# Kernel optimization log

Hardware: AMD Instinct MI355X
Metric: run time of the kernel (lower is better)

The kernel has to match this reference:

```python
import jax, jax.numpy as jnp
import numpy as np
import math
from itertools import combinations

SEQ_LEN = 8
D_MODEL = 2048
OUT_DIM = 1152
WAY = 5
SHOT = 5
N_SUPPORT = WAY * SHOT
N_QUERIES = 200
TUPLES = np.array(list(combinations(range(SEQ_LEN), 2)), dtype=np.int32)  # [28, 2]
L = TUPLES.shape[0]  # 28 temporal tuples
PE_SCALE = 0.1
LN_EPS = 1e-5
COS_EPS = 1e-8


def _pos_encoding(seq, d):
    pos = jnp.arange(seq, dtype=jnp.float32)[:, None]
    div = jnp.exp(jnp.arange(0, d, 2, dtype=jnp.float32) * (-math.log(10000.0) / d))
    pe = jnp.zeros((seq, d), dtype=jnp.float32)
    pe = pe.at[:, 0::2].set(jnp.sin(pos * div) * PE_SCALE)
    pe = pe.at[:, 1::2].set(jnp.cos(pos * div) * PE_SCALE)
    return pe  # [seq, d]


def _layernorm(x, g, b):
    mu = x.mean(-1, keepdims=True)
    var = ((x - mu) ** 2).mean(-1, keepdims=True)
    return (x - mu) * jax.lax.rsqrt(var + LN_EPS) * g + b


def setup_inputs() -> dict:
    key = jax.random.key(0)
    ks = jax.random.split(key, 6)
    support_set = jax.random.normal(ks[0], (N_SUPPORT, SEQ_LEN, D_MODEL), jnp.float32)
    queries = jax.random.normal(ks[1], (N_QUERIES, SEQ_LEN, D_MODEL), jnp.float32)
    # sorted equal-shot episode: labels = [0]*5 + [1]*5 + ... + [4]*5
    support_labels = jnp.repeat(jnp.arange(WAY, dtype=jnp.int32), SHOT)
    k_w = jax.random.normal(ks[2], (OUT_DIM, 2 * D_MODEL), jnp.float32) * 0.02
    v_w = jax.random.normal(ks[3], (OUT_DIM, 2 * D_MODEL), jnp.float32) * 0.02
    k_b = jnp.zeros((OUT_DIM,), jnp.float32)
    v_b = jnp.zeros((OUT_DIM,), jnp.float32)
    ln_k_g = jnp.ones((OUT_DIM,), jnp.float32)
    ln_k_b = jnp.zeros((OUT_DIM,), jnp.float32)
    return {"support_set": support_set, "support_labels": support_labels,
            "queries": queries, "k_w": k_w, "k_b": k_b, "v_w": v_w, "v_b": v_b,
            "ln_k_g": ln_k_g, "ln_k_b": ln_k_b}


def reference(support_set, support_labels, queries, k_w, k_b, v_w, v_b, ln_k_g, ln_k_b):
    # dropout is inference-mode (identity)
    pe = _pos_encoding(SEQ_LEN, D_MODEL)
    sp = support_set + pe  # [Ns, S, D_MODEL]
    qp = queries + pe      # [Nq, S, D_MODEL]

    tup = jnp.asarray(TUPLES)
    # gather temporal tuples: [N, L, 2, D_MODEL] -> [N, L, 2*D_MODEL]
    s_t = sp[:, tup].reshape(N_SUPPORT, L, 2 * D_MODEL)
    q_t = qp[:, tup].reshape(N_QUERIES, L, 2 * D_MODEL)

    ks_s = _layernorm(s_t @ k_w.T + k_b, ln_k_g, ln_k_b)  # [Ns, L, OUT]
    ks_q = _layernorm(q_t @ k_w.T + k_b, ln_k_g, ln_k_b)  # [Nq, L, OUT]
    vs_s = s_t @ v_w.T + v_b                               # [Ns, L, OUT] (no norm, per original)
    vs_q = q_t @ v_w.T + v_b                               # [Nq, L, OUT]

    # labels are sorted equal-shot -> group by class via reshape
    ks_c = ks_s.reshape(WAY, SHOT, L, OUT_DIM)
    vs_c = vs_s.reshape(WAY, SHOT, L, OUT_DIM)

    # attention scores: [WAY, Nq, L(query tuple), SHOT, L(support tuple)]
    scores = jnp.einsum('qld,wsed->wqlse', ks_q, ks_c) / math.sqrt(OUT_DIM)
    attn = jax.nn.softmax(scores.reshape(WAY, N_QUERIES, L, SHOT * L), axis=-1)
    attn = attn.reshape(WAY, N_QUERIES, L, SHOT, L)
    # prototype: sum over shot of attn @ class_v -> [WAY, Nq, L, OUT]
    proto = jnp.einsum('wqlse,wsed->wqld', attn, vs_c)

    # query logits: -||q_v - proto||_F^2 / L per class
    diff = vs_q[None] - proto  # [WAY, Nq, L, OUT]
    ori = (-(diff ** 2).sum(axis=(-2, -1)) / L).T  # [Nq, WAY]

    # all_distances_tensor [Nq, L*OUT, WAY]
    A = jnp.transpose(proto, (1, 2, 3, 0)).reshape(N_QUERIES, L * OUT_DIM, WAY)
    num = jnp.einsum('qda,qdb->qab', A, A)            # [Nq, WAY, WAY]
    nrm = jnp.sqrt((A * A).sum(axis=1))               # [Nq, WAY]
    den = jnp.maximum(nrm[:, :, None] * nrm[:, None, :], COS_EPS)
    sim = num / den                                    # [Nq, WAY, WAY]
    return sim, ori
```

## Files before the change

kernel.cpp:

```cpp
#include <hip/hip_runtime.h>
#include <hip/hip_bf16.h>
#include <math.h>

typedef __hip_bfloat16 bf16;
typedef short s16x8 __attribute__((ext_vector_type(8)));
typedef float f32x4 __attribute__((ext_vector_type(4)));

#define NQ 200
#define SEQ 8
#define DM 2048
#define OUTD 1152
#define LT 28
#define M_ALL 6300
#define SM 5600
#define SN_PAD 768
#define ATT_STRIDE 720
#define N2 2304
#define KP 160
#define CH_Q 50
#define CH_ROWS 1400
#define CH_MPAD 1408
#define ABLK 144

__device__ __forceinline__ float bf2f(bf16 v) { return __bfloat162float(v); }
__device__ __forceinline__ bf16 f2bf(float v) { return __float2bfloat16(v); }
__device__ __forceinline__ float ubits2f(unsigned int u16) {
    unsigned int i = u16 << 16;
    float f; __builtin_memcpy(&f, &i, 4); return f;
}
__device__ __forceinline__ unsigned short f2bits(float f) {
    bf16 b = __float2bfloat16(f);
    unsigned short u; __builtin_memcpy(&u, &b, 2); return u;
}

__device__ const int TUP_A[LT] = {0,0,0,0,0,0,0,1,1,1,1,1,1,2,2,2,2,2,3,3,3,3,4,4,4,5,5,6};
__device__ const int TUP_B[LT] = {1,2,3,4,5,6,7,2,3,4,5,6,7,3,4,5,6,7,4,5,6,7,5,6,7,6,7,7};

__global__ __launch_bounds__(256) void wconv2_k(const float4* __restrict__ kw,
                                                const float4* __restrict__ vw,
                                                ushort4* __restrict__ o) {
    int i = blockIdx.x * 256 + threadIdx.x;
    float4 v = (i < 1179648) ? kw[i] : vw[i - 1179648];
    ushort4 r;
    r.x = f2bits(v.x); r.y = f2bits(v.y); r.z = f2bits(v.z); r.w = f2bits(v.w);
    o[i] = r;
}

__global__ __launch_bounds__(256) void pe_k(float* __restrict__ pe,
                                            bf16* __restrict__ attn_tail) {
    int i = blockIdx.x * 256 + threadIdx.x;
    int s = i >> 11, d = i & 2047;
    float dv = expf((float)(d & ~1) * (-9.210340371976184f / 2048.0f));
    float ang = (float)s * dv;
    pe[i] = (d & 1) ? cosf(ang) * 0.1f : sinf(ang) * 0.1f;
    for (int j = i; j < 32 * ATT_STRIDE; j += 64 * 256) attn_tail[j] = f2bf(0.f);
}

__global__ __launch_bounds__(256) void pex_k(const float* __restrict__ sup,
                                             const float* __restrict__ qry,
                                             const float* __restrict__ pe,
                                             bf16* __restrict__ pexb) {
    int r = blockIdx.x, t = threadIdx.x;
    int n, s;
    const float* src;
    if (r < 200) { n = r >> 3; s = r & 7; src = sup; }
    else { int rr = r - 200; n = rr >> 3; s = rr & 7; src = qry; }
    const float4* row = (const float4*)(src + ((size_t)n * SEQ + s) * DM);
    const float4* per = (const float4*)(pe + (size_t)s * DM);
    ushort4* orow = (ushort4*)(pexb + (size_t)r * DM);
    for (int d = t; d < DM / 4; d += 256) {
        float4 a = row[d], p = per[d];
        ushort4 o;
        o.x = f2bits(a.x + p.x); o.y = f2bits(a.y + p.y);
        o.z = f2bits(a.z + p.z); o.w = f2bits(a.w + p.w);
        orow[d] = o;
    }
}

__global__ __launch_bounds__(256) void gemm_bt(
    const bf16* __restrict__ A, int lda, size_t aZ,
    const bf16* __restrict__ B, int ldb, size_t bZ,
    float scale, bf16* __restrict__ C, int ldc, size_t cZ, int K, int mlim) {
    const int gx = gridDim.x, gy = gridDim.y;
    const int nwg = gx * gy * (int)gridDim.z;
    const int orig = ((int)blockIdx.z * gy + blockIdx.y) * gx + blockIdx.x;
    const int qc = nwg >> 3, rc = nwg & 7;
    const int xcd = orig & 7, sub = orig >> 3;
    const int lg = (xcd < rc ? xcd * (qc + 1) : rc * (qc + 1) + (xcd - rc) * qc) + sub;
    const int bx = lg % gx;
    const int rest = lg / gx;
    const int by = rest % gy, bz = rest / gy;

    const unsigned short* Ag0 = (const unsigned short*)A + aZ * bz;
    const unsigned short* Bg0 = (const unsigned short*)B + bZ * bz;
    const size_t cbase = cZ * bz;
    const int tile_m = bx * 128, tile_n = by * 128;
    __shared__ unsigned short As[4 * 128 * 8];
    __shared__ unsigned short Bs[4 * 128 * 8];
    const int t = threadIdx.x, lane = t & 63, wave = t >> 6;
    const int wm = (wave & 1) * 64, wn = (wave >> 1) * 64;
    const int srow = t >> 1, sq0 = (t & 1) * 2;
    const unsigned short* Ag = Ag0 + (size_t)(tile_m + srow) * lda + (t & 1) * 16;
    const unsigned short* Bg = Bg0 + (size_t)(tile_n + srow) * ldb + (t & 1) * 16;
    unsigned short* AsW0 = &As[((sq0 + 0) * 128 + srow) * 8];
    unsigned short* AsW1 = &As[((sq0 + 1) * 128 + srow) * 8];
    unsigned short* BsW0 = &Bs[((sq0 + 0) * 128 + srow) * 8];
    unsigned short* BsW1 = &Bs[((sq0 + 1) * 128 + srow) * 8];
    const int fr = lane & 15, quad = lane >> 4;

    f32x4 acc[4][4];
#pragma unroll
    for (int i = 0; i < 4; i++)
#pragma unroll
        for (int j = 0; j < 4; j++) acc[i][j] = {0.f, 0.f, 0.f, 0.f};

    for (int k0 = 0; k0 < K; k0 += 32) {
        uint4 a0 = *(const uint4*)(Ag + k0);
        uint4 a1 = *(const uint4*)(Ag + k0 + 8);
        uint4 b0 = *(const uint4*)(Bg + k0);
        uint4 b1 = *(const uint4*)(Bg + k0 + 8);
        __syncthreads();
        *(uint4*)AsW0 = a0; *(uint4*)AsW1 = a1;
        *(uint4*)BsW0 = b0; *(uint4*)BsW1 = b1;
        __syncthreads();
        s16x8 af[4], bfv[4];
#pragma unroll
        for (int i = 0; i < 4; i++)
            af[i] = *(const s16x8*)&As[(quad * 128 + wm + i * 16 + fr) * 8];
#pragma unroll
        for (int j = 0; j < 4; j++)
            bfv[j] = *(const s16x8*)&Bs[(quad * 128 + wn + j * 16 + fr) * 8];
#pragma unroll
        for (int i = 0; i < 4; i++)
#pragma unroll
            for (int j = 0; j < 4; j++)
                acc[i][j] = __builtin_amdgcn_mfma_f32_16x16x32_bf16(af[i], bfv[j], acc[i][j], 0, 0, 0);
    }

    const int rb = quad * 4;
#pragma unroll
    for (int i = 0; i < 4; i++)
#pragma unroll
        for (int j = 0; j < 4; j++) {
            const int col = tile_n + wn + j * 16 + fr;
#pragma unroll
            for (int r = 0; r < 4; r++) {
                const int row = tile_m + wm + i * 16 + rb + r;
                if (row < mlim)
                    C[cbase + (size_t)row * ldc + col] = f2bf(acc[i][j][r] * scale);
            }
        }
}

__global__ __launch_bounds__(256) void combine_k(
    const unsigned int* __restrict__ Yk, const float* __restrict__ kb,
    const float* __restrict__ lng, const float* __restrict__ lnb,
    bf16* __restrict__ ks) {
    const int m = blockIdx.x, t = threadIdx.x, lane = t & 63, wave = t >> 6;
    int mm = m < 700 ? m : m - 700;
    int base = m < 700 ? 0 : 200;
    int nsamp = mm / LT, l = mm - nsamp * LT;
    const unsigned int* ya = Yk + (size_t)(base + nsamp * 8 + TUP_A[l]) * (N2 / 2);
    const unsigned int* yb = Yk + (size_t)(base + nsamp * 8 + TUP_B[l]) * (N2 / 2);
    float vals[5];
    int cnt = 0;
    float s = 0.f, s2 = 0.f;
    for (int n = t; n < OUTD; n += 256) {
        unsigned int ua = ya[n], ub = yb[n];
        float vk = ubits2f(ua & 0xFFFFu) + ubits2f(ub >> 16) + kb[n];
        vals[cnt++] = vk;
        s += vk; s2 += vk * vk;
    }
    for (int o = 32; o > 0; o >>= 1) { s += __shfl_xor(s, o); s2 += __shfl_xor(s2, o); }
    __shared__ float r1[4], r2[4];
    if (lane == 0) { r1[wave] = s; r2[wave] = s2; }
    __syncthreads();
    s = r1[0] + r1[1] + r1[2] + r1[3];
    s2 = r2[0] + r2[1] + r2[2] + r2[3];
    float mu = s * (1.f / OUTD);
    float var = s2 * (1.f / OUTD) - mu * mu;
    float inv = rsqrtf(fmaxf(var, 0.f) + 1e-5f);
    cnt = 0;
    for (int n = t; n < OUTD; n += 256)
        ks[(size_t)m * OUTD + n] = f2bf((vals[cnt++] - mu) * inv * lng[n] + lnb[n]);
}

__global__ __launch_bounds__(256) void combine_v(
    const unsigned int* __restrict__ Yv, const float* __restrict__ vb,
    bf16* __restrict__ vs) {
    const int m = blockIdx.x, t = threadIdx.x;
    int mm = m < 700 ? m : m - 700;
    int base = m < 700 ? 0 : 200;
    int nsamp = mm / LT, l = mm - nsamp * LT;
    const unsigned int* ya = Yv + (size_t)(base + nsamp * 8 + TUP_A[l]) * (N2 / 2);
    const unsigned int* yb = Yv + (size_t)(base + nsamp * 8 + TUP_B[l]) * (N2 / 2);
    for (int n = t; n < OUTD; n += 256) {
        unsigned int ua = ya[n], ub = yb[n];
        vs[(size_t)m * OUTD + n] =
            f2bf(ubits2f(ua & 0xFFFFu) + ubits2f(ub >> 16) + vb[n]);
    }
}

__global__ __launch_bounds__(320) void softmax_k(const bf16* __restrict__ sc,
                                                 bf16* __restrict__ attn) {
    const int row = blockIdx.x, w = threadIdx.x >> 6, lane = threadIdx.x & 63;
    const bf16* src = sc + (size_t)row * SN_PAD + w * 140;
    bf16* dst = attn + (size_t)row * ATT_STRIDE + w * ABLK;
    float a = bf2f(src[lane]);
    float b = bf2f(src[lane + 64]);
    float c = (lane < 12) ? bf2f(src[lane + 128]) : -3.0e38f;
    float m = fmaxf(fmaxf(a, b), c);
    for (int o = 32; o > 0; o >>= 1) m = fmaxf(m, __shfl_xor(m, o));
    float ea = __expf(a - m), eb = __expf(b - m);
    float ec = (lane < 12) ? __expf(c - m) : 0.f;
    float s = ea + eb + ec;
    for (int o = 32; o > 0; o >>= 1) s += __shfl_xor(s, o);
    float inv = 1.f / s;
    dst[lane] = f2bf(ea * inv);
    dst[lane + 64] = f2bf(eb * inv);
    if (lane < 16) dst[lane + 128] = f2bf(lane < 12 ? ec * inv : 0.f);
}

__global__ __launch_bounds__(256) void vspad_k(const bf16* __restrict__ vs,
                                               bf16* __restrict__ vp,
                                               float* __restrict__ gbuf) {
    int idx = blockIdx.x * 256 + threadIdx.x;
    if (blockIdx.x == 0)
        for (int i = threadIdx.x; i < NQ * 21; i += 256) gbuf[i] = 0.f;
    if (idx >= 5 * OUTD * KP) return;
    int j = idx % KP;
    int rest = idx / KP;
    int dcol = rest % OUTD;
    int w = rest / OUTD;
    vp[idx] = (j < 140) ? vs[(size_t)(w * 140 + j) * OUTD + dcol] : f2bf(0.f);
}

__global__ __launch_bounds__(256) void gramred_k(const bf16* __restrict__ protoc,
                                                 const bf16* __restrict__ vs,
                                                 float* __restrict__ gbuf,
                                                 int row0, int q0) {
    const int ql = blockIdx.x;
    const int lgb = blockIdx.y;
    const int t = threadIdx.x, lane = t & 63, wave = t >> 6;
    const size_t PZ = (size_t)CH_MPAD * OUTD;
    float g[15] = {0.f};
    float h[5] = {0.f, 0.f, 0.f, 0.f, 0.f};
    float e = 0.f;
    for (int idx = t; idx < 2 * OUTD / 8; idx += 256) {
        int li = idx / 144;
        int dv = idx - li * 144;
        int l = lgb * 2 + li;
        size_t ml = (size_t)(ql * LT + l) * OUTD + dv * 8;
        s16x8 pw0 = *(const s16x8*)&protoc[0 * PZ + ml];
        s16x8 pw1 = *(const s16x8*)&protoc[1 * PZ + ml];
        s16x8 pw2 = *(const s16x8*)&protoc[2 * PZ + ml];
        s16x8 pw3 = *(const s16x8*)&protoc[3 * PZ + ml];
        s16x8 pw4 = *(const s16x8*)&protoc[4 * PZ + ml];
        s16x8 vv = *(const s16x8*)&vs[(size_t)(700 + row0 + ql * LT + l) * OUTD + dv * 8];
#pragma unroll
        for (int ee = 0; ee < 8; ee++) {
            float pv[5];
            pv[0] = ubits2f((unsigned short)pw0[ee]);
            pv[1] = ubits2f((unsigned short)pw1[ee]);
            pv[2] = ubits2f((unsigned short)pw2[ee]);
            pv[3] = ubits2f((unsigned short)pw3[ee]);
            pv[4] = ubits2f((unsigned short)pw4[ee]);
            float v = ubits2f((unsigned short)vv[ee]);
            e += v * v;
            int c = 0;
#pragma unroll
            for (int a = 0; a < 5; a++) {
                h[a] += v * pv[a];
#pragma unroll
                for (int b = a; b < 5; b++) g[c++] += pv[a] * pv[b];
            }
        }
    }
    float vals[21];
#pragma unroll
    for (int k = 0; k < 15; k++) vals[k] = g[k];
#pragma unroll
    for (int k = 0; k < 5; k++) vals[15 + k] = h[k];
    vals[20] = e;
#pragma unroll
    for (int k = 0; k < 21; k++)
        for (int o = 32; o > 0; o >>= 1) vals[k] += __shfl_xor(vals[k], o);
    __shared__ float red[4][21];
    if (lane == 0)
#pragma unroll
        for (int k = 0; k < 21; k++) red[wave][k] = vals[k];
    __syncthreads();
    if (t < 21) {
        float s = red[0][t] + red[1][t] + red[2][t] + red[3][t];
        atomicAdd(&gbuf[(q0 + ql) * 21 + t], s);
    }
}

__global__ __launch_bounds__(64) void out_k(const float* __restrict__ gbuf,
                                            float* __restrict__ out) {
    int q = blockIdx.x;
    if (threadIdx.x != 0) return;
    const float* r = gbuf + q * 21;
    float G[5][5];
    int c = 0;
    for (int a = 0; a < 5; a++)
        for (int b = a; b < 5; b++) { G[a][b] = r[c]; G[b][a] = r[c]; c++; }
    float e = r[20];
    float nrm[5];
    for (int a = 0; a < 5; a++) nrm[a] = sqrtf(fmaxf(G[a][a], 0.f));
    for (int a = 0; a < 5; a++)
        for (int b = 0; b < 5; b++)
            out[(size_t)q * 25 + a * 5 + b] = G[a][b] / fmaxf(nrm[a] * nrm[b], 1e-8f);
    for (int w = 0; w < 5; w++)
        out[5000 + (size_t)q * 5 + w] = -(e - 2.f * r[15 + w] + G[w][w]) * (1.f / 28.f);
}

extern "C" void kernel_launch(void* const* d_in, const int* in_sizes, int n_in,
                              void* d_out, int out_size, void* d_ws, size_t ws_size,
                              hipStream_t stream) {
    const float* sup = (const float*)d_in[0];
    const float* qry = (const float*)d_in[2];
    const float* k_w = (const float*)d_in[3];
    const float* k_b = (const float*)d_in[4];
    const float* v_w = (const float*)d_in[5];
    const float* v_b = (const float*)d_in[6];
    const float* lng = (const float*)d_in[7];
    const float* lnb = (const float*)d_in[8];
    (void)in_sizes; (void)n_in; (void)out_size; (void)ws_size;

    char* ws = (char*)d_ws;
    bf16* pexb   = (bf16*)(ws + 0);
    bf16* wbf    = (bf16*)(ws + 7864320);
    bf16* Yk     = (bf16*)(ws + 26738688);
    bf16* Yv     = (bf16*)(ws + 35033088);
    bf16* ks     = (bf16*)(ws + 0);
    bf16* vs     = (bf16*)(ws + 16220160);
    bf16* sc     = (bf16*)(ws + 30735360);
    bf16* vsp    = (bf16*)(ws + 39386112);
    bf16* attn   = (bf16*)(ws + 41229312);
    float* gbuf  = (float*)(ws + 49339392);
    float* pe    = (float*)(ws + 49356192);
    bf16* protoc = (bf16*)(ws + 0);

    pe_k<<<dim3(64), dim3(256), 0, stream>>>(pe, attn + (size_t)SM * ATT_STRIDE);
    pex_k<<<dim3(1800), dim3(256), 0, stream>>>(sup, qry, pe, pexb);
    wconv2_k<<<dim3(9216), dim3(256), 0, stream>>>(
        (const float4*)k_w, (const float4*)v_w, (ushort4*)wbf);

    gemm_bt<<<dim3(15, 18, 2), dim3(256), 0, stream>>>(
        pexb, DM, 0, wbf, DM, (size_t)4718592,
        1.0f, Yk, N2, (size_t)4147200, DM, 1800);

    combine_k<<<dim3(M_ALL), dim3(256), 0, stream>>>(
        (const unsigned int*)Yk, k_b, lng, lnb, ks);
    combine_v<<<dim3(M_ALL), dim3(256), 0, stream>>>(
        (const unsigned int*)Yv, v_b, vs);

    gemm_bt<<<dim3(44, 6, 1), dim3(256), 0, stream>>>(
        ks + (size_t)700 * OUTD, OUTD, 0, ks, OUTD, 0,
        0.029462782549439484f, sc, SN_PAD, 0, OUTD, 5632);

    vspad_k<<<dim3((5 * OUTD * KP + 255) / 256), dim3(256), 0, stream>>>(
        vs, vsp, gbuf);
    softmax_k<<<dim3(SM), dim3(320), 0, stream>>>(sc, attn);

    for (int c = 0; c < 4; c++) {
        gemm_bt<<<dim3(11, 9, 5), dim3(256), 0, stream>>>(
            attn + (size_t)c * CH_ROWS * ATT_STRIDE, ATT_STRIDE, (size_t)ABLK,
            vsp, KP, (size_t)OUTD * KP,
            1.0f, protoc, OUTD, (size_t)CH_MPAD * OUTD, KP, CH_MPAD);
        gramred_k<<<dim3(CH_Q, 14), dim3(256), 0, stream>>>(
            protoc, vs, gbuf, c * CH_ROWS, c * CH_Q);
    }

    out_k<<<dim3(NQ), dim3(64), 0, stream>>>(gbuf, (float*)d_out);
}
```

Before: 339.1 us.

## Template GEMM on N-tile width, use 64-wide tiles, merge small elementwise kernels

Makes the bf16 MFMA GEMM a template over the N-tile width and launches all GEMMs with 128x64 tiles, doubling the grid so more workgroups fill the CUs. It also merges combine_k and combine_v into one launch and folds vspad into the softmax kernel, cutting launch overhead. Narrower tiles lower per-block data reuse and add redundant A-tile loads.

```diff
diff --git a/kernel.cpp b/kernel.cpp
--- a/kernel.cpp
+++ b/kernel.cpp
@@ -77,10 +77,12 @@
     }
 }
 
+template <int TN>
 __global__ __launch_bounds__(256) void gemm_bt(
     const bf16* __restrict__ A, int lda, size_t aZ,
     const bf16* __restrict__ B, int ldb, size_t bZ,
     float scale, bf16* __restrict__ C, int ldc, size_t cZ, int K, int mlim) {
+    constexpr int JN = TN / 32;
     const int gx = gridDim.x, gy = gridDim.y;
     const int nwg = gx * gy * (int)gridDim.z;
     const int orig = ((int)blockIdx.z * gy + blockIdx.y) * gx + blockIdx.x;
@@ -94,46 +96,56 @@
     const unsigned short* Ag0 = (const unsigned short*)A + aZ * bz;
     const unsigned short* Bg0 = (const unsigned short*)B + bZ * bz;
     const size_t cbase = cZ * bz;
-    const int tile_m = bx * 128, tile_n = by * 128;
+    const int tile_m = bx * 128, tile_n = by * TN;
     __shared__ unsigned short As[4 * 128 * 8];
-    __shared__ unsigned short Bs[4 * 128 * 8];
+    __shared__ unsigned short Bs[4 * TN * 8];
     const int t = threadIdx.x, lane = t & 63, wave = t >> 6;
-    const int wm = (wave & 1) * 64, wn = (wave >> 1) * 64;
+    const int wm = (wave & 1) * 64, wn = (wave >> 1) * (TN / 2);
     const int srow = t >> 1, sq0 = (t & 1) * 2;
     const unsigned short* Ag = Ag0 + (size_t)(tile_m + srow) * lda + (t & 1) * 16;
-    const unsigned short* Bg = Bg0 + (size_t)(tile_n + srow) * ldb + (t & 1) * 16;
     unsigned short* AsW0 = &As[((sq0 + 0) * 128 + srow) * 8];
     unsigned short* AsW1 = &As[((sq0 + 1) * 128 + srow) * 8];
-    unsigned short* BsW0 = &Bs[((sq0 + 0) * 128 + srow) * 8];
-    unsigned short* BsW1 = &Bs[((sq0 + 1) * 128 + srow) * 8];
+    const unsigned short* Bg;
+    unsigned short* BsW0;
+    unsigned short* BsW1 = nullptr;
+    if constexpr (TN == 128) {
+        Bg = Bg0 + (size_t)(tile_n + srow) * ldb + (t & 1) * 16;
+        BsW0 = &Bs[((sq0 + 0) * 128 + srow) * 8];
+        BsW1 = &Bs[((sq0 + 1) * 128 + srow) * 8];
+    } else {
+        Bg = Bg0 + (size_t)(tile_n + (t >> 2)) * ldb + (t & 3) * 8;
+        BsW0 = &Bs[((t & 3) * 64 + (t >> 2)) * 8];
+    }
     const int fr = lane & 15, quad = lane >> 4;
 
-    f32x4 acc[4][4];
+    f32x4 acc[4][JN];
 #pragma unroll
     for (int i = 0; i < 4; i++)
 #pragma unroll
-        for (int j = 0; j < 4; j++) acc[i][j] = {0.f, 0.f, 0.f, 0.f};
+        for (int j = 0; j < JN; j++) acc[i][j] = {0.f, 0.f, 0.f, 0.f};
 
     for (int k0 = 0; k0 < K; k0 += 32) {
         uint4 a0 = *(const uint4*)(Ag + k0);
         uint4 a1 = *(const uint4*)(Ag + k0 + 8);
         uint4 b0 = *(const uint4*)(Bg + k0);
-        uint4 b1 = *(const uint4*)(Bg + k0 + 8);
+        uint4 b1;
+        if constexpr (TN == 128) b1 = *(const uint4*)(Bg + k0 + 8);
         __syncthreads();
         *(uint4*)AsW0 = a0; *(uint4*)AsW1 = a1;
-        *(uint4*)BsW0 = b0; *(uint4*)BsW1 = b1;
+        *(uint4*)BsW0 = b0;
+        if constexpr (TN == 128) *(uint4*)BsW1 = b1;
         __syncthreads();
-        s16x8 af[4], bfv[4];
+        s16x8 af[4], bfv[JN];
 #pragma unroll
         for (int i = 0; i < 4; i++)
             af[i] = *(const s16x8*)&As[(quad * 128 + wm + i * 16 + fr) * 8];
 #pragma unroll
-        for (int j = 0; j < 4; j++)
-            bfv[j] = *(const s16x8*)&Bs[(quad * 128 + wn + j * 16 + fr) * 8];
+        for (int j = 0; j < JN; j++)
+            bfv[j] = *(const s16x8*)&Bs[(quad * TN + wn + j * 16 + fr) * 8];
 #pragma unroll
         for (int i = 0; i < 4; i++)
 #pragma unroll
-            for (int j = 0; j < 4; j++)
+            for (int j = 0; j < JN; j++)
                 acc[i][j] = __builtin_amdgcn_mfma_f32_16x16x32_bf16(af[i], bfv[j], acc[i][j], 0, 0, 0);
     }
 
@@ -141,7 +153,7 @@
 #pragma unroll
     for (int i = 0; i < 4; i++)
 #pragma unroll
-        for (int j = 0; j < 4; j++) {
+        for (int j = 0; j < JN; j++) {
             const int col = tile_n + wn + j * 16 + fr;
 #pragma unroll
             for (int r = 0; r < 4; r++) {
@@ -152,16 +164,29 @@
         }
 }
 
-__global__ __launch_bounds__(256) void combine_k(
-    const unsigned int* __restrict__ Yk, const float* __restrict__ kb,
+__global__ __launch_bounds__(256) void combine_kv(
+    const unsigned int* __restrict__ Yk, const unsigned int* __restrict__ Yv,
+    const float* __restrict__ kb, const float* __restrict__ vb,
     const float* __restrict__ lng, const float* __restrict__ lnb,
-    bf16* __restrict__ ks) {
-    const int m = blockIdx.x, t = threadIdx.x, lane = t & 63, wave = t >> 6;
+    bf16* __restrict__ ks, bf16* __restrict__ vs) {
+    const int t = threadIdx.x, lane = t & 63, wave = t >> 6;
+    int m = blockIdx.x;
+    const bool vpath = m >= M_ALL;
+    if (vpath) m -= M_ALL;
     int mm = m < 700 ? m : m - 700;
     int base = m < 700 ? 0 : 200;
     int nsamp = mm / LT, l = mm - nsamp * LT;
-    const unsigned int* ya = Yk + (size_t)(base + nsamp * 8 + TUP_A[l]) * (N2 / 2);
-    const unsigned int* yb = Yk + (size_t)(base + nsamp * 8 + TUP_B[l]) * (N2 / 2);
+    const unsigned int* Y = vpath ? Yv : Yk;
+    const unsigned int* ya = Y + (size_t)(base + nsamp * 8 + TUP_A[l]) * (N2 / 2);
+    const unsigned int* yb = Y + (size_t)(base + nsamp * 8 + TUP_B[l]) * (N2 / 2);
+    if (vpath) {
+        for (int n = t; n < OUTD; n += 256) {
+            unsigned int ua = ya[n], ub = yb[n];
+            vs[(size_t)m * OUTD + n] =
+                f2bf(ubits2f(ua & 0xFFFFu) + ubits2f(ub >> 16) + vb[n]);
+        }
+        return;
+    }
     float vals[5];
     int cnt = 0;
     float s = 0.f, s2 = 0.f;
@@ -185,49 +210,35 @@
         ks[(size_t)m * OUTD + n] = f2bf((vals[cnt++] - mu) * inv * lng[n] + lnb[n]);
 }
 
-__global__ __launch_bounds__(256) void combine_v(
-    const unsigned int* __restrict__ Yv, const float* __restrict__ vb,
-    bf16* __restrict__ vs) {
-    const int m = blockIdx.x, t = threadIdx.x;
-    int mm = m < 700 ? m : m - 700;
-    int base = m < 700 ? 0 : 200;
-    int nsamp = mm / LT, l = mm - nsamp * LT;
-    const unsigned int* ya = Yv + (size_t)(base + nsamp * 8 + TUP_A[l]) * (N2 / 2);
-    const unsigned int* yb = Yv + (size_t)(base + nsamp * 8 + TUP_B[l]) * (N2 / 2);
-    for (int n = t; n < OUTD; n += 256) {
-        unsigned int ua = ya[n], ub = yb[n];
-        vs[(size_t)m * OUTD + n] =
-            f2bf(ubits2f(ua & 0xFFFFu) + ubits2f(ub >> 16) + vb[n]);
-    }
-}
-
-__global__ __launch_bounds__(320) void softmax_k(const bf16* __restrict__ sc,
-                                                 bf16* __restrict__ attn) {
-    const int row = blockIdx.x, w = threadIdx.x >> 6, lane = threadIdx.x & 63;
-    const bf16* src = sc + (size_t)row * SN_PAD + w * 140;
-    bf16* dst = attn + (size_t)row * ATT_STRIDE + w * ABLK;
-    float a = bf2f(src[lane]);
-    float b = bf2f(src[lane + 64]);
-    float c = (lane < 12) ? bf2f(src[lane + 128]) : -3.0e38f;
-    float m = fmaxf(fmaxf(a, b), c);
-    for (int o = 32; o > 0; o >>= 1) m = fmaxf(m, __shfl_xor(m, o));
-    float ea = __expf(a - m), eb = __expf(b - m);
-    float ec = (lane < 12) ? __expf(c - m) : 0.f;
-    float s = ea + eb + ec;
-    for (int o = 32; o > 0; o >>= 1) s += __shfl_xor(s, o);
-    float inv = 1.f / s;
-    dst[lane] = f2bf(ea * inv);
-    dst[lane + 64] = f2bf(eb * inv);
-    if (lane < 16) dst[lane + 128] = f2bf(lane < 12 ? ec * inv : 0.f);
-}
-
-__global__ __launch_bounds__(256) void vspad_k(const bf16* __restrict__ vs,
-                                               bf16* __restrict__ vp,
-                                               float* __restrict__ gbuf) {
-    int idx = blockIdx.x * 256 + threadIdx.x;
-    if (blockIdx.x == 0)
-        for (int i = threadIdx.x; i < NQ * 21; i += 256) gbuf[i] = 0.f;
-    if (idx >= 5 * OUTD * KP) return;
+__global__ __launch_bounds__(320) void sv_k(const bf16* __restrict__ sc,
+                                            bf16* __restrict__ attn,
+                                            const bf16* __restrict__ vs,
+                                            bf16* __restrict__ vp,
+                                            float* __restrict__ gbuf) {
+    const int t = threadIdx.x;
+    if (blockIdx.x < SM) {
+        const int row = blockIdx.x, w = t >> 6, lane = t & 63;
+        const bf16* src = sc + (size_t)row * SN_PAD + w * 140;
+        bf16* dst = attn + (size_t)row * ATT_STRIDE + w * ABLK;
+        float a = bf2f(src[lane]);
+        float b = bf2f(src[lane + 64]);
+        float c = (lane < 12) ? bf2f(src[lane + 128]) : -3.0e38f;
+        float m = fmaxf(fmaxf(a, b), c);
+        for (int o = 32; o > 0; o >>= 1) m = fmaxf(m, __shfl_xor(m, o));
+        float ea = __expf(a - m), eb = __expf(b - m);
+        float ec = (lane < 12) ? __expf(c - m) : 0.f;
+        float s = ea + eb + ec;
+        for (int o = 32; o > 0; o >>= 1) s += __shfl_xor(s, o);
+        float inv = 1.f / s;
+        dst[lane] = f2bf(ea * inv);
+        dst[lane + 64] = f2bf(eb * inv);
+        if (lane < 16) dst[lane + 128] = f2bf(lane < 12 ? ec * inv : 0.f);
+        return;
+    }
+    const int vb = blockIdx.x - SM;
+    if (vb == 0)
+        for (int i = t; i < NQ * 21; i += 320) gbuf[i] = 0.f;
+    int idx = vb * 320 + t;
     int j = idx % KP;
     int rest = idx / KP;
     int dcol = rest % OUTD;
@@ -347,25 +358,22 @@
     wconv2_k<<<dim3(9216), dim3(256), 0, stream>>>(
         (const float4*)k_w, (const float4*)v_w, (ushort4*)wbf);
 
-    gemm_bt<<<dim3(15, 18, 2), dim3(256), 0, stream>>>(
+    gemm_bt<64><<<dim3(15, 36, 2), dim3(256), 0, stream>>>(
         pexb, DM, 0, wbf, DM, (size_t)4718592,
         1.0f, Yk, N2, (size_t)4147200, DM, 1800);
 
-    combine_k<<<dim3(M_ALL), dim3(256), 0, stream>>>(
-        (const unsigned int*)Yk, k_b, lng, lnb, ks);
-    combine_v<<<dim3(M_ALL), dim3(256), 0, stream>>>(
-        (const unsigned int*)Yv, v_b, vs);
-
-    gemm_bt<<<dim3(44, 6, 1), dim3(256), 0, stream>>>(
+    combine_kv<<<dim3(2 * M_ALL), dim3(256), 0, stream>>>(
+        (const unsigned int*)Yk, (const unsigned int*)Yv,
+        k_b, v_b, lng, lnb, ks, vs);
+
+    gemm_bt<64><<<dim3(44, 12, 1), dim3(256), 0, stream>>>(
         ks + (size_t)700 * OUTD, OUTD, 0, ks, OUTD, 0,
         0.029462782549439484f, sc, SN_PAD, 0, OUTD, 5632);
 
-    vspad_k<<<dim3((5 * OUTD * KP + 255) / 256), dim3(256), 0, stream>>>(
-        vs, vsp, gbuf);
-    softmax_k<<<dim3(SM), dim3(320), 0, stream>>>(sc, attn);
+    sv_k<<<dim3(SM + 2880), dim3(320), 0, stream>>>(sc, attn, vs, vsp, gbuf);
 
     for (int c = 0; c < 4; c++) {
-        gemm_bt<<<dim3(11, 9, 5), dim3(256), 0, stream>>>(
+        gemm_bt<64><<<dim3(11, 18, 5), dim3(256), 0, stream>>>(
             attn + (size_t)c * CH_ROWS * ATT_STRIDE, ATT_STRIDE, (size_t)ABLK,
             vsp, KP, (size_t)OUTD * KP,
             1.0f, protoc, OUTD, (size_t)CH_MPAD * OUTD, KP, CH_MPAD);
```

Measured after the change: 334.8 us. About the same (-1.3%).
